# Optimization experiments

Measured on AMD Instinct MI355X. Metric: run time of the kernel, lower is better.

## Reference

```python
import jax, jax.numpy as jnp
import numpy as np

B, N, DIM = 4, 2048, 256
HEADS, CODEBOOK, HD = 4, 8192, 64  # HD = DIM // HEADS


def setup_inputs() -> dict:
    key = jax.random.key(0)
    k1, k2 = jax.random.split(key)
    x = jax.random.normal(k1, (B, N, DIM), dtype=jnp.float32)
    embed = jax.random.normal(k2, (HEADS, CODEBOOK, HD), dtype=jnp.float32)
    return {"x": x, "embed": embed}


def reference(x, embed):
    b, n, dim = x.shape
    h, c, d = embed.shape
    # 'b n (h d) -> h b n d' then pack to 'h (b n) d'
    flat = x.reshape(b, n, h, d).transpose(2, 0, 1, 3).reshape(h, b * n, d)
    x2 = jnp.sum(flat * flat, axis=-1)              # [h, bn]
    y2 = jnp.sum(embed * embed, axis=-1)            # [h, c]
    xy = jnp.einsum('hmd,hcd->hmc', flat, embed)    # [h, bn, c]
    sq = x2[:, :, None] + y2[:, None, :] - 2.0 * xy
    dist = -jnp.sqrt(jnp.maximum(sq, 0.0))          # clamp for fp safety
    embed_ind = jnp.argmax(dist, axis=-1)           # [h, bn]
    # gather codes per head
    quantize = jnp.take_along_axis(embed, embed_ind[:, :, None], axis=1)  # [h, bn, d]
    # 'h (b n) d -> b n (h d)'
    quantize = quantize.reshape(h, b, n, d).transpose(1, 2, 0, 3).reshape(b, n, h * d)
    # 'h (b n) -> b n h'
    embed_ind = embed_ind.reshape(h, b, n).transpose(1, 2, 0)
    return quantize, embed_ind
```

## Files before the change

### kernel.cpp

```cpp
#include <hip/hip_runtime.h>
#include <hip/hip_bf16.h>


#define HEADS    4
#define CODEBOOK 8192
#define HD       64
#define BQ       8192
#define QOFF     (4 * 2048 * 256)
#define NPART    8
#define CPART    (CODEBOOK / NPART)
#define SCODES   64
#define NSTAGE   (CPART / SCODES)
#define RSCALE   4096.0f
#define RINV     (1.0f / 4096.0f)

typedef _Float16 f16x8 __attribute__((ext_vector_type(8)));
typedef float    f32x4 __attribute__((ext_vector_type(4)));

__device__ unsigned long long g_best[HEADS * BQ];
__device__ int                g_cnt[HEADS * 32];

__device__ inline void split2(float f, _Float16& h0, _Float16& h1) {
    h0 = (_Float16)f;
    float r = f - (float)h0;
    h1 = (_Float16)(r * RSCALE);
}

__device__ inline unsigned sortable(float v) {
    unsigned s = __float_as_uint(v);
    return s ^ ((s & 0x80000000u) ? 0xFFFFFFFFu : 0x80000000u);
}

__global__ __launch_bounds__(256, 2) void dist_kernel(const float* __restrict__ x,
                                                      const float* __restrict__ embed,
                                                      float* __restrict__ out) {
    __shared__ __align__(16) _Float16 tile[2][2][SCODES * 64];
    __shared__ float y2s[CPART];
    __shared__ int s_old;

    const int bid  = blockIdx.x;
    const int part = bid & 7;
    const int qg   = (bid >> 3) & 31;
    const int h    = bid >> 8;
    const int t    = threadIdx.x;
    const int wave = t >> 6;
    const int lane = t & 63;
    const int col  = lane & 15;
    const int quad = lane >> 4;

    const int qbase = qg * 256 + wave * 64;
    const int cbase = part * CPART;

    f16x8 a[4][2][2];
#pragma unroll
    for (int rt = 0; rt < 4; rt++) {
#pragma unroll
        for (int kh = 0; kh < 2; kh++) {
            const float* p = x + ((size_t)(qbase + rt * 16 + col) * 256 + h * 64 + kh * 32 + quad * 8);
#pragma unroll
            for (int j = 0; j < 8; j++) {
                _Float16 h0, h1;
                split2(p[j], h0, h1);
                a[rt][0][kh][j] = h0;
                a[rt][1][kh][j] = h1;
            }
        }
    }

    const float* esrc = embed + ((size_t)h * CODEBOOK + cbase) * HD + (size_t)t * 8;
    const int row  = t >> 3;
    const int gsw  = (t & 7) ^ (row & 7);
    const int ldA  = row * 64 + gsw * 8;
    const int ldB  = (row + 32) * 64 + gsw * 8;

    float bv[4][4]; int bc[4][4];
#pragma unroll
    for (int rt = 0; rt < 4; rt++)
#pragma unroll
        for (int r = 0; r < 4; r++) { bv[rt][r] = -3.4e38f; bc[rt][r] = 0; }

    float4 pfA0, pfA1, pfB0, pfB1;

    auto stage_write = [&](int buf, int stage) {
        float fA[8] = {pfA0.x, pfA0.y, pfA0.z, pfA0.w, pfA1.x, pfA1.y, pfA1.z, pfA1.w};
        float fB[8] = {pfB0.x, pfB0.y, pfB0.z, pfB0.w, pfB1.x, pfB1.y, pfB1.z, pfB1.w};
        f16x8 vA0, vA1, vB0, vB1;
        float ssA = 0.f, ssB = 0.f;
#pragma unroll
        for (int j = 0; j < 8; j++) {
            _Float16 h0, h1;
            split2(fA[j], h0, h1);
            vA0[j] = h0; vA1[j] = h1;
            ssA = fmaf(fA[j], fA[j], ssA);
            split2(fB[j], h0, h1);
            vB0[j] = h0; vB1[j] = h1;
            ssB = fmaf(fB[j], fB[j], ssB);
        }
        *reinterpret_cast<f16x8*>(&tile[buf][0][ldA]) = vA0;
        *reinterpret_cast<f16x8*>(&tile[buf][1][ldA]) = vA1;
        *reinterpret_cast<f16x8*>(&tile[buf][0][ldB]) = vB0;
        *reinterpret_cast<f16x8*>(&tile[buf][1][ldB]) = vB1;
#pragma unroll
        for (int off = 4; off >= 1; off >>= 1) {
            ssA += __shfl_xor(ssA, off, 8);
            ssB += __shfl_xor(ssB, off, 8);
        }
        if ((t & 7) == 0) {
            y2s[stage * SCODES + row]      = -0.5f * ssA;
            y2s[stage * SCODES + row + 32] = -0.5f * ssB;
        }
    };
    auto stage_load = [&](int stage) {
        const float* ps = esrc + (size_t)stage * (SCODES * HD);
        pfA0 = *reinterpret_cast<const float4*>(ps);
        pfA1 = *reinterpret_cast<const float4*>(ps + 4);
        pfB0 = *reinterpret_cast<const float4*>(ps + 32 * HD);
        pfB1 = *reinterpret_cast<const float4*>(ps + 32 * HD + 4);
    };

    stage_load(0);
    stage_write(0, 0);
    stage_load(1);
    __syncthreads();

    const int swbase = col & 7;
    const f32x4 z4 = {0.f, 0.f, 0.f, 0.f};

    for (int s = 0; s < NSTAGE; s++) {
        if (s + 1 < NSTAGE) stage_write((s + 1) & 1, s + 1);
        if (s + 2 < NSTAGE) stage_load(s + 2);

#pragma unroll
        for (int inner = 0; inner < 4; inner++) {
            const int rbase = (inner * 16 + col) * 64;
            f16x8 b[2][2];
#pragma unroll
            for (int lvl = 0; lvl < 2; lvl++)
#pragma unroll
                for (int kh = 0; kh < 2; kh++)
                    b[lvl][kh] = *reinterpret_cast<const f16x8*>(
                        &tile[s & 1][lvl][rbase + ((((kh << 2) | quad) ^ swbase) << 3)]);

            const int   c   = s * SCODES + inner * 16 + col;
            const float ycn = y2s[c];
#pragma unroll
            for (int rt = 0; rt < 4; rt++) {
                __builtin_amdgcn_s_setprio(1);
                f32x4 aA = __builtin_amdgcn_mfma_f32_16x16x32_f16(a[rt][0][0], b[0][0], z4, 0, 0, 0);
                f32x4 aB = __builtin_amdgcn_mfma_f32_16x16x32_f16(a[rt][0][0], b[1][0], z4, 0, 0, 0);
                aB = __builtin_amdgcn_mfma_f32_16x16x32_f16(a[rt][1][0], b[0][0], aB, 0, 0, 0);
                aA = __builtin_amdgcn_mfma_f32_16x16x32_f16(a[rt][0][1], b[0][1], aA, 0, 0, 0);
                aB = __builtin_amdgcn_mfma_f32_16x16x32_f16(a[rt][0][1], b[1][1], aB, 0, 0, 0);
                aB = __builtin_amdgcn_mfma_f32_16x16x32_f16(a[rt][1][1], b[0][1], aB, 0, 0, 0);
                __builtin_amdgcn_s_setprio(0);
#pragma unroll
                for (int r = 0; r < 4; r++) {
                    float sv = fmaf(aB[r], RINV, aA[r] + ycn);
                    if (sv > bv[rt][r]) { bv[rt][r] = sv; bc[rt][r] = c; }
                }
            }
        }
        __syncthreads();
    }

#pragma unroll
    for (int rt = 0; rt < 4; rt++) {
#pragma unroll
        for (int r = 0; r < 4; r++) {
            float v = bv[rt][r]; int c = bc[rt][r];
#pragma unroll
            for (int off = 8; off >= 1; off >>= 1) {
                float ov = __shfl_xor(v, off, 16); int oc = __shfl_xor(c, off, 16);
                if (ov > v || (ov == v && oc < c)) { v = ov; c = oc; }
            }
            if (col == 0) {
                int q = h * BQ + qbase + rt * 16 + quad * 4 + r;
                unsigned long long pk =
                    ((unsigned long long)sortable(v) << 32) | (unsigned)(~(cbase + c));
                atomicMax(&g_best[q], pk);
            }
        }
    }

    const int grp = (h << 5) | qg;
    __syncthreads();
    if (t == 0) s_old = atomicAdd(&g_cnt[grp], 1);
    __syncthreads();
    if (s_old != NPART - 1) return;

    if (t == 0) atomicExch(&g_cnt[grp], 0);

    int* sidx = reinterpret_cast<int*>(y2s);
    const int m0 = qg * 256;
    {
        const int q = h * BQ + m0 + t;
        unsigned long long pk = atomicAdd(&g_best[q], 0ull);
        int mc = (int)(~(unsigned)pk) & (CODEBOOK - 1);
        out[QOFF + (size_t)(m0 + t) * 4 + h] = (float)mc;
        sidx[t] = mc;
    }
    __syncthreads();

    const int rr = lane >> 4;
    const int fo = (lane & 15) * 4;
#pragma unroll
    for (int i = 0; i < 16; i++) {
        const int r   = wave * 64 + i * 4 + rr;
        const int idx = sidx[r];
        const float4 v = *reinterpret_cast<const float4*>(
            embed + ((size_t)h * CODEBOOK + idx) * HD + fo);
        *reinterpret_cast<float4*>(out + (size_t)(m0 + r) * 256 + h * 64 + fo) = v;
    }
}

extern "C" void kernel_launch(void* const* d_in, const int* in_sizes, int n_in,
                              void* d_out, int out_size, void* d_ws, size_t ws_size,
                              hipStream_t stream) {
    const float* x     = (const float*)d_in[0];
    const float* embed = (const float*)d_in[1];
    float*       out   = (float*)d_out;

    dist_kernel<<<1024, 256, 0, stream>>>(x, embed, out);
}
```

Before: 176.2 us.

## Precompute split fp16 codebook in a prep kernel and stream tiles via global_load_lds

Adds a prep kernel that splits the fp32 codebook once into hi/lo fp16 arrays and precomputes the per-code squared norms in global memory. Previously each of the 32 query-group blocks per partition redid this conversion. The distance kernel now loads the prepared fp16 tiles directly into shared memory with asynchronous global_load_lds, which removes the register staging and per-stage conversion arithmetic, and it reads y2 from global memory. The cost is an extra kernel launch and a global round-trip for the prepared data, and the code relies on the async LDS loads being complete at the existing barriers.

Result: no change. 176.6 us, median of 4 (+0.2%).

```diff
diff --git a/kernel.cpp b/kernel.cpp
--- a/kernel.cpp
+++ b/kernel.cpp
@@ -1,5 +1,4 @@
 #include <hip/hip_runtime.h>
-#include <hip/hip_bf16.h>
 
 
 #define HEADS    4
@@ -17,6 +16,9 @@
 typedef _Float16 f16x8 __attribute__((ext_vector_type(8)));
 typedef float    f32x4 __attribute__((ext_vector_type(4)));
 
+__device__ _Float16 g_e0[HEADS * CODEBOOK * HD];
+__device__ _Float16 g_e1[HEADS * CODEBOOK * HD];
+__device__ float    g_y2[HEADS * CODEBOOK];
 __device__ unsigned long long g_best[HEADS * BQ];
 __device__ int                g_cnt[HEADS * 32];
 
@@ -31,11 +33,41 @@
     return s ^ ((s & 0x80000000u) ? 0xFFFFFFFFu : 0x80000000u);
 }
 
+__device__ inline void gl_lds16(const void* g, void* l) {
+    __builtin_amdgcn_global_load_lds(
+        (const __attribute__((address_space(1))) void*)g,
+        (__attribute__((address_space(3))) void*)l, 16, 0, 0);
+}
+
+__global__ __launch_bounds__(256) void prep_kernel(const float* __restrict__ embed) {
+    const int t   = threadIdx.x;
+    const int row = blockIdx.x * 32 + (t >> 3);
+    const int g   = t & 7;
+    const float* p = embed + (size_t)row * HD + g * 8;
+    float f[8];
+    *reinterpret_cast<float4*>(&f[0]) = *reinterpret_cast<const float4*>(p);
+    *reinterpret_cast<float4*>(&f[4]) = *reinterpret_cast<const float4*>(p + 4);
+    f16x8 v0, v1;
+    float ss = 0.f;
+#pragma unroll
+    for (int j = 0; j < 8; j++) {
+        _Float16 h0, h1;
+        split2(f[j], h0, h1);
+        v0[j] = h0; v1[j] = h1;
+        ss = fmaf(f[j], f[j], ss);
+    }
+    *reinterpret_cast<f16x8*>(&g_e0[(size_t)row * HD + g * 8]) = v0;
+    *reinterpret_cast<f16x8*>(&g_e1[(size_t)row * HD + g * 8]) = v1;
+#pragma unroll
+    for (int off = 4; off >= 1; off >>= 1)
+        ss += __shfl_xor(ss, off, 8);
+    if (g == 0) g_y2[row] = -0.5f * ss;
+}
+
 __global__ __launch_bounds__(256, 2) void dist_kernel(const float* __restrict__ x,
                                                       const float* __restrict__ embed,
                                                       float* __restrict__ out) {
-    __shared__ __align__(16) _Float16 tile[2][2][SCODES * 64];
-    __shared__ float y2s[CPART];
+    __shared__ __align__(16) _Float16 tile[2][2][SCODES * HD];
     __shared__ int s_old;
 
     const int bid  = blockIdx.x;
@@ -51,88 +83,55 @@
     const int qbase = qg * 256 + wave * 64;
     const int cbase = part * CPART;
 
+    const int p  = wave & 1;
+    const int hh = wave >> 1;
+    const _Float16* eb   = p ? g_e1 : g_e0;
+    const _Float16* gsrc = eb
+        + ((size_t)(h * CODEBOOK + cbase + hh * 32 + (lane >> 3))) * HD
+        + ((lane & 7) ^ (lane >> 3)) * 8;
+    auto stage_issue = [&](int st, int buf) {
+        const _Float16* src = gsrc + (size_t)st * (SCODES * HD);
+#pragma unroll
+        for (int i = 0; i < 4; i++)
+            gl_lds16(src + i * 8 * HD, &tile[buf][p][(hh * 32 + i * 8) * HD]);
+    };
+    const float* y2p = g_y2 + h * CODEBOOK + cbase;
+
+    stage_issue(0, 0);
+
     f16x8 a[4][2][2];
 #pragma unroll
     for (int rt = 0; rt < 4; rt++) {
 #pragma unroll
         for (int kh = 0; kh < 2; kh++) {
-            const float* p = x + ((size_t)(qbase + rt * 16 + col) * 256 + h * 64 + kh * 32 + quad * 8);
+            const float* xp = x + ((size_t)(qbase + rt * 16 + col) * 256 + h * 64 + kh * 32 + quad * 8);
 #pragma unroll
             for (int j = 0; j < 8; j++) {
                 _Float16 h0, h1;
-                split2(p[j], h0, h1);
+                split2(xp[j], h0, h1);
                 a[rt][0][kh][j] = h0;
                 a[rt][1][kh][j] = h1;
             }
         }
     }
 
-    const float* esrc = embed + ((size_t)h * CODEBOOK + cbase) * HD + (size_t)t * 8;
-    const int row  = t >> 3;
-    const int gsw  = (t & 7) ^ (row & 7);
-    const int ldA  = row * 64 + gsw * 8;
-    const int ldB  = (row + 32) * 64 + gsw * 8;
-
     float bv[4][4]; int bc[4][4];
 #pragma unroll
     for (int rt = 0; rt < 4; rt++)
 #pragma unroll
         for (int r = 0; r < 4; r++) { bv[rt][r] = -3.4e38f; bc[rt][r] = 0; }
 
-    float4 pfA0, pfA1, pfB0, pfB1;
-
-    auto stage_write = [&](int buf, int stage) {
-        float fA[8] = {pfA0.x, pfA0.y, pfA0.z, pfA0.w, pfA1.x, pfA1.y, pfA1.z, pfA1.w};
-        float fB[8] = {pfB0.x, pfB0.y, pfB0.z, pfB0.w, pfB1.x, pfB1.y, pfB1.z, pfB1.w};
-        f16x8 vA0, vA1, vB0, vB1;
-        float ssA = 0.f, ssB = 0.f;
-#pragma unroll
-        for (int j = 0; j < 8; j++) {
-            _Float16 h0, h1;
-            split2(fA[j], h0, h1);
-            vA0[j] = h0; vA1[j] = h1;
-            ssA = fmaf(fA[j], fA[j], ssA);
-            split2(fB[j], h0, h1);
-            vB0[j] = h0; vB1[j] = h1;
-            ssB = fmaf(fB[j], fB[j], ssB);
-        }
-        *reinterpret_cast<f16x8*>(&tile[buf][0][ldA]) = vA0;
-        *reinterpret_cast<f16x8*>(&tile[buf][1][ldA]) = vA1;
-        *reinterpret_cast<f16x8*>(&tile[buf][0][ldB]) = vB0;
-        *reinterpret_cast<f16x8*>(&tile[buf][1][ldB]) = vB1;
-#pragma unroll
-        for (int off = 4; off >= 1; off >>= 1) {
-            ssA += __shfl_xor(ssA, off, 8);
-            ssB += __shfl_xor(ssB, off, 8);
-        }
-        if ((t & 7) == 0) {
-            y2s[stage * SCODES + row]      = -0.5f * ssA;
-            y2s[stage * SCODES + row + 32] = -0.5f * ssB;
-        }
-    };
-    auto stage_load = [&](int stage) {
-        const float* ps = esrc + (size_t)stage * (SCODES * HD);
-        pfA0 = *reinterpret_cast<const float4*>(ps);
-        pfA1 = *reinterpret_cast<const float4*>(ps + 4);
-        pfB0 = *reinterpret_cast<const float4*>(ps + 32 * HD);
-        pfB1 = *reinterpret_cast<const float4*>(ps + 32 * HD + 4);
-    };
-
-    stage_load(0);
-    stage_write(0, 0);
-    stage_load(1);
     __syncthreads();
 
     const int swbase = col & 7;
     const f32x4 z4 = {0.f, 0.f, 0.f, 0.f};
 
     for (int s = 0; s < NSTAGE; s++) {
-        if (s + 1 < NSTAGE) stage_write((s + 1) & 1, s + 1);
-        if (s + 2 < NSTAGE) stage_load(s + 2);
+        if (s + 1 < NSTAGE) stage_issue(s + 1, (s + 1) & 1);
 
 #pragma unroll
         for (int inner = 0; inner < 4; inner++) {
-            const int rbase = (inner * 16 + col) * 64;
+            const int rbase = (inner * 16 + col) * HD;
             f16x8 b[2][2];
 #pragma unroll
             for (int lvl = 0; lvl < 2; lvl++)
@@ -141,8 +140,9 @@
                     b[lvl][kh] = *reinterpret_cast<const f16x8*>(
                         &tile[s & 1][lvl][rbase + ((((kh << 2) | quad) ^ swbase) << 3)]);
 
-            const int   c   = s * SCODES + inner * 16 + col;
-            const float ycn = y2s[c];
+            const int   cl  = inner * 16 + col;
+            const int   c   = s * SCODES + cl;
+            const float ycn = y2p[c];
 #pragma unroll
             for (int rt = 0; rt < 4; rt++) {
                 __builtin_amdgcn_s_setprio(1);
@@ -190,7 +190,7 @@
 
     if (t == 0) atomicExch(&g_cnt[grp], 0);
 
-    int* sidx = reinterpret_cast<int*>(y2s);
+    int* sidx = reinterpret_cast<int*>(tile);
     const int m0 = qg * 256;
     {
         const int q = h * BQ + m0 + t;
@@ -220,5 +220,6 @@
     const float* embed = (const float*)d_in[1];
     float*       out   = (float*)d_out;
 
+    prep_kernel<<<1024, 256, 0, stream>>>(embed);
     dist_kernel<<<1024, 256, 0, stream>>>(x, embed, out);
 }
```
